# Performance work log

Measured on AMD Instinct MI355X. Metric: run time of the kernel, lower is better.

## Reference

```python
import jax, jax.numpy as jnp
import numpy as np

N_NODES = 128
N_EDGES = N_NODES * (N_NODES - 1)  # fully-connected, no self-loops
N_IN = 128
N_HID = 256
N_OUT = 128
BATCH = 32


def _build_rel_matrices():
    # one-hot incidence matrices for fully-connected off-diagonal graph
    send_idx, recv_idx = [], []
    for i in range(N_NODES):
        for j in range(N_NODES):
            if i != j:
                send_idx.append(i)
                recv_idx.append(j)
    eye = np.eye(N_NODES, dtype=np.float32)
    rel_send = eye[np.asarray(send_idx)]  # [E, N]
    rel_rec = eye[np.asarray(recv_idx)]   # [E, N]
    return jnp.asarray(rel_rec), jnp.asarray(rel_send)


def setup_inputs() -> dict:
    key = jax.random.key(0)
    k = jax.random.split(key, 6)
    rel_rec, rel_send = _build_rel_matrices()
    s1 = 1.0 / np.sqrt(2 * N_IN)
    s2 = 1.0 / np.sqrt(N_HID)
    return {
        "x": jax.random.normal(k[0], (BATCH, N_NODES, N_IN), dtype=jnp.float32),
        "rel_type": jax.random.uniform(k[1], (BATCH, N_EDGES, 4), dtype=jnp.float32),
        "rel_rec": rel_rec,
        "rel_send": rel_send,
        "W1": jax.random.normal(k[2], (2 * N_IN, N_HID), dtype=jnp.float32) * s1,
        "b1": jnp.zeros((N_HID,), dtype=jnp.float32),
        "W2": jax.random.normal(k[3], (N_HID, N_OUT), dtype=jnp.float32) * s2,
        "b2": jnp.zeros((N_OUT,), dtype=jnp.float32),
    }


def reference(x, rel_type, rel_rec, rel_send, W1, b1, W2, b2):
    # node2edge: gather sender/receiver node features via incidence matmuls
    senders = jnp.einsum('en,bnf->bef', rel_send, x)    # [B, E, n_in]
    receivers = jnp.einsum('en,bnf->bef', rel_rec, x)   # [B, E, n_in]
    edges = jnp.concatenate([senders, receivers], axis=-1)  # [B, E, 2*n_in]
    # 2-layer MLP on edges (rel_type is unused in the original forward)
    h = jax.nn.relu(edges @ W1 + b1)
    msg = h @ W2 + b2                                   # [B, E, n_out]
    # edge2node: scatter-sum then normalize by in-degree
    agg = jnp.einsum('en,bef->bnf', rel_rec, msg)       # [B, N, n_out]
    norm = rel_rec.sum(axis=0)[None, :, None]           # [1, N, 1]
    return agg / (norm + 1e-6)
```

## Files before the change

### kernel.cpp

```cpp
#include <hip/hip_runtime.h>

#define BATCH 32
#define NN    128
#define NIN   128
#define NHID  256
#define NOUT  128
#define ROWS  (BATCH * NN)

__global__ __launch_bounds__(256) void k1_sr(
    const float* __restrict__ x, const float* __restrict__ W1,
    const float* __restrict__ b1, float* __restrict__ S, float* __restrict__ R)
{
    __shared__ float xr[8][128];
    const int row0 = blockIdx.x * 8;
    const int t = threadIdx.x;
    for (int idx = t; idx < 8 * 128; idx += 256)
        xr[idx >> 7][idx & 127] = x[(size_t)row0 * NIN + idx];
    __syncthreads();

    const int c = t;
    float accs[8], accr[8];
#pragma unroll
    for (int r = 0; r < 8; ++r) { accs[r] = 0.f; accr[r] = 0.f; }

    for (int k = 0; k < NIN; k += 4) {
        float wa[4], wb[4];
#pragma unroll
        for (int kk = 0; kk < 4; ++kk) {
            wa[kk] = W1[(size_t)(k + kk) * NHID + c];
            wb[kk] = W1[(size_t)(NIN + k + kk) * NHID + c];
        }
#pragma unroll
        for (int r = 0; r < 8; ++r) {
            const float4 xv = *(const float4*)(&xr[r][k]);
            accs[r] = fmaf(xv.w, wa[3], fmaf(xv.z, wa[2], fmaf(xv.y, wa[1], fmaf(xv.x, wa[0], accs[r]))));
            accr[r] = fmaf(xv.w, wb[3], fmaf(xv.z, wb[2], fmaf(xv.y, wb[1], fmaf(xv.x, wb[0], accr[r]))));
        }
    }
    const float bias = b1[c];
#pragma unroll
    for (int r = 0; r < 8; ++r) {
        S[(size_t)(row0 + r) * NHID + c] = accs[r];
        R[(size_t)(row0 + r) * NHID + c] = accr[r] + bias;
    }
}

__global__ __launch_bounds__(256) void k2_g(
    const float* __restrict__ S, const float* __restrict__ R, float* __restrict__ G)
{
    const int blk = blockIdx.x;
    const int b   = blk >> 4;
    const int nt  = (blk >> 2) & 3;
    const int cc  = blk & 3;
    const int c0  = cc * 64;

    __shared__ float s_lds[128][64];
    const int t  = threadIdx.x;
    const int cl = t & 63;
    const int ng = t >> 6;

    for (int idx = t; idx < 128 * 64; idx += 256) {
        const int i = idx >> 6, c = idx & 63;
        s_lds[i][c] = S[((size_t)(b * NN + i)) * NHID + c0 + c];
    }
    __syncthreads();

    const int n0 = nt * 32 + ng * 8;
    float rv[8], acc[8];
#pragma unroll
    for (int q = 0; q < 8; ++q) {
        rv[q]  = R[((size_t)(b * NN + n0 + q)) * NHID + c0 + cl];
        acc[q] = 0.f;
    }

    for (int i = 0; i < 128; ++i) {
        const float s = s_lds[i][cl];
#pragma unroll
        for (int q = 0; q < 8; ++q)
            acc[q] += fmaxf(s + rv[q], 0.f);
    }

#pragma unroll
    for (int q = 0; q < 8; ++q) {
        const float self = fmaxf(s_lds[n0 + q][cl] + rv[q], 0.f);
        G[((size_t)(b * NN + n0 + q)) * NHID + c0 + cl] = acc[q] - self;
    }
}

__global__ __launch_bounds__(256) void k3_out(
    const float* __restrict__ G, const float* __restrict__ W2,
    const float* __restrict__ b2, float* __restrict__ out)
{
    __shared__ float g[16][256];
    const int row0 = blockIdx.x * 16;
    const int t = threadIdx.x;
    for (int idx = t; idx < 16 * 256; idx += 256)
        g[idx >> 8][idx & 255] = G[(size_t)row0 * NHID + idx];
    __syncthreads();

    const int c  = t & 127;
    const int rh = t >> 7;
    float acc[8];
#pragma unroll
    for (int r = 0; r < 8; ++r) acc[r] = 0.f;

    for (int k = 0; k < NHID; k += 4) {
        float w[4];
#pragma unroll
        for (int kk = 0; kk < 4; ++kk)
            w[kk] = W2[(size_t)(k + kk) * NOUT + c];
#pragma unroll
        for (int r = 0; r < 8; ++r) {
            const float4 gv = *(const float4*)(&g[rh * 8 + r][k]);
            acc[r] = fmaf(gv.w, w[3], fmaf(gv.z, w[2], fmaf(gv.y, w[1], fmaf(gv.x, w[0], acc[r]))));
        }
    }
    const float inv  = 1.0f / (127.0f + 1e-6f);
    const float bias = 127.0f * b2[c];
#pragma unroll
    for (int r = 0; r < 8; ++r)
        out[(size_t)(row0 + rh * 8 + r) * NOUT + c] = (acc[r] + bias) * inv;
}

extern "C" void kernel_launch(void* const* d_in, const int* in_sizes, int n_in,
                              void* d_out, int out_size, void* d_ws, size_t ws_size,
                              hipStream_t stream)
{
    const float* x  = (const float*)d_in[0];
    const float* W1 = (const float*)d_in[4];
    const float* b1 = (const float*)d_in[5];
    const float* W2 = (const float*)d_in[6];
    const float* b2 = (const float*)d_in[7];
    float* out = (float*)d_out;

    float* S = (float*)d_ws;
    float* R = S + (size_t)ROWS * NHID;
    float* G = R + (size_t)ROWS * NHID;

    k1_sr <<<ROWS / 8,        256, 0, stream>>>(x, W1, b1, S, R);
    k2_g  <<<BATCH * 4 * 4,   256, 0, stream>>>(S, R, G);
    k3_out<<<ROWS / 16,       256, 0, stream>>>(G, W2, b2, out);
}
```

Before: 119.7 us.

## Fuse relu-sum aggregation with output projection into single kernel

```diff
diff --git a/kernel.cpp b/kernel.cpp
--- a/kernel.cpp
+++ b/kernel.cpp
@@ -45,81 +45,74 @@
     }
 }
 
-__global__ __launch_bounds__(256) void k2_g(
-    const float* __restrict__ S, const float* __restrict__ R, float* __restrict__ G)
+__global__ __launch_bounds__(512) void k2_fused(
+    const float* __restrict__ S, const float* __restrict__ R,
+    const float* __restrict__ W2, const float* __restrict__ b2,
+    float* __restrict__ out)
 {
+    __shared__ float smem[128 * 256];
+
     const int blk = blockIdx.x;
-    const int b   = blk >> 4;
-    const int nt  = (blk >> 2) & 3;
-    const int cc  = blk & 3;
-    const int c0  = cc * 64;
+    const int b   = blk >> 3;
+    const int nt  = blk & 7;
+    const int n0  = nt * 16;
 
-    __shared__ float s_lds[128][64];
-    const int t  = threadIdx.x;
-    const int cl = t & 63;
-    const int ng = t >> 6;
+    const int t = threadIdx.x;
+    const int c = t & 255;
+    const int h = t >> 8;
 
-    for (int idx = t; idx < 128 * 64; idx += 256) {
-        const int i = idx >> 6, c = idx & 63;
-        s_lds[i][c] = S[((size_t)(b * NN + i)) * NHID + c0 + c];
-    }
+    const float4* Sv  = (const float4*)(S + (size_t)b * NN * NHID);
+    float4*       sm4 = (float4*)smem;
+#pragma unroll
+    for (int it = 0; it < 16; ++it)
+        sm4[t + it * 512] = Sv[t + it * 512];
     __syncthreads();
 
-    const int n0 = nt * 32 + ng * 8;
+    const int r0 = n0 + h * 8;
     float rv[8], acc[8];
 #pragma unroll
     for (int q = 0; q < 8; ++q) {
-        rv[q]  = R[((size_t)(b * NN + n0 + q)) * NHID + c0 + cl];
+        rv[q]  = R[((size_t)(b * NN + r0 + q)) * NHID + c];
         acc[q] = 0.f;
     }
 
-    for (int i = 0; i < 128; ++i) {
-        const float s = s_lds[i][cl];
+#pragma unroll 4
+    for (int i = 0; i < NN; ++i) {
+        const float s = smem[i * NHID + c];
 #pragma unroll
         for (int q = 0; q < 8; ++q)
             acc[q] += fmaxf(s + rv[q], 0.f);
     }
+#pragma unroll
+    for (int q = 0; q < 8; ++q)
+        acc[q] -= fmaxf(smem[(r0 + q) * NHID + c] + rv[q], 0.f);
 
+    __syncthreads();
 #pragma unroll
-    for (int q = 0; q < 8; ++q) {
-        const float self = fmaxf(s_lds[n0 + q][cl] + rv[q], 0.f);
-        G[((size_t)(b * NN + n0 + q)) * NHID + c0 + cl] = acc[q] - self;
-    }
-}
-
-__global__ __launch_bounds__(256) void k3_out(
-    const float* __restrict__ G, const float* __restrict__ W2,
-    const float* __restrict__ b2, float* __restrict__ out)
-{
-    __shared__ float g[16][256];
-    const int row0 = blockIdx.x * 16;
-    const int t = threadIdx.x;
-    for (int idx = t; idx < 16 * 256; idx += 256)
-        g[idx >> 8][idx & 255] = G[(size_t)row0 * NHID + idx];
+    for (int q = 0; q < 8; ++q)
+        smem[(h * 8 + q) * NHID + c] = acc[q];
     __syncthreads();
 
-    const int c  = t & 127;
-    const int rh = t >> 7;
-    float acc[8];
-#pragma unroll
-    for (int r = 0; r < 8; ++r) acc[r] = 0.f;
+    const int co = t & 127;
+    const int rg = t >> 7;
+    float acc3[4] = {0.f, 0.f, 0.f, 0.f};
 
     for (int k = 0; k < NHID; k += 4) {
         float w[4];
 #pragma unroll
         for (int kk = 0; kk < 4; ++kk)
-            w[kk] = W2[(size_t)(k + kk) * NOUT + c];
+            w[kk] = W2[(size_t)(k + kk) * NOUT + co];
 #pragma unroll
-        for (int r = 0; r < 8; ++r) {
-            const float4 gv = *(const float4*)(&g[rh * 8 + r][k]);
-            acc[r] = fmaf(gv.w, w[3], fmaf(gv.z, w[2], fmaf(gv.y, w[1], fmaf(gv.x, w[0], acc[r]))));
+        for (int r = 0; r < 4; ++r) {
+            const float4 gv = *(const float4*)(&smem[(rg * 4 + r) * NHID + k]);
+            acc3[r] = fmaf(gv.w, w[3], fmaf(gv.z, w[2], fmaf(gv.y, w[1], fmaf(gv.x, w[0], acc3[r]))));
         }
     }
     const float inv  = 1.0f / (127.0f + 1e-6f);
-    const float bias = 127.0f * b2[c];
+    const float bias = 127.0f * b2[co];
 #pragma unroll
-    for (int r = 0; r < 8; ++r)
-        out[(size_t)(row0 + rh * 8 + r) * NOUT + c] = (acc[r] + bias) * inv;
+    for (int r = 0; r < 4; ++r)
+        out[((size_t)(b * NN + n0 + rg * 4 + r)) * NOUT + co] = (acc3[r] + bias) * inv;
 }
 
 extern "C" void kernel_launch(void* const* d_in, const int* in_sizes, int n_in,
@@ -135,9 +128,7 @@
 
     float* S = (float*)d_ws;
     float* R = S + (size_t)ROWS * NHID;
-    float* G = R + (size_t)ROWS * NHID;
 
-    k1_sr <<<ROWS / 8,        256, 0, stream>>>(x, W1, b1, S, R);
-    k2_g  <<<BATCH * 4 * 4,   256, 0, stream>>>(S, R, G);
-    k3_out<<<ROWS / 16,       256, 0, stream>>>(G, W2, b2, out);
+    k1_sr   <<<ROWS / 8,     256, 0, stream>>>(x, W1, b1, S, R);
+    k2_fused<<<BATCH * 8,    512, 0, stream>>>(S, R, W2, b2, out);
 }
```

Measured after the change: 116.0 us. 3.1% less time.
